# Optimization experiments

Hardware: AMD Instinct MI355X
Metric: run time of the kernel (lower is better)

Reference implementation:

```python
import jax, jax.numpy as jnp
import numpy as np


def _rel_coords_log(ws: int) -> np.ndarray:
    # matches torch.meshgrid default indexing='ij'
    idx = np.arange(ws, dtype=np.float32)
    coords = np.stack(np.meshgrid(idx, idx, indexing='ij'), axis=0).reshape(2, -1)  # [2, ws^2]
    rel = coords[:, :, None] - coords[:, None, :]  # [2, T, T]
    rel = rel.transpose(1, 2, 0).reshape(-1, 2)    # [T*T, 2]
    return np.sign(rel) * np.log1p(np.abs(rel))


def setup_inputs() -> dict:
    key = jax.random.key(0)
    ks = jax.random.split(key, 9)
    B, C, Hd, ws, meta_h = 256, 256, 8, 16, 256
    s = 1.0 / np.sqrt(C)
    return {
        'x': jax.random.normal(ks[0], (B, C, ws, ws), dtype=jnp.float32),
        'w_qkv': jax.random.normal(ks[1], (3 * C, C), dtype=jnp.float32) * s,
        'b_qkv': jax.random.normal(ks[2], (3 * C,), dtype=jnp.float32) * 0.01,
        'w_proj': jax.random.normal(ks[3], (C, C), dtype=jnp.float32) * s,
        'b_proj': jax.random.normal(ks[4], (C,), dtype=jnp.float32) * 0.01,
        'mw1': jax.random.normal(ks[5], (meta_h, 2), dtype=jnp.float32) * 0.5,
        'mb1': jax.random.normal(ks[6], (meta_h,), dtype=jnp.float32) * 0.01,
        'mw2': jax.random.normal(ks[7], (Hd, meta_h), dtype=jnp.float32) * (1.0 / np.sqrt(meta_h)),
        'mb2': jax.random.normal(ks[8], (Hd,), dtype=jnp.float32) * 0.01,
        'tau': jnp.ones((1, Hd, 1, 1), dtype=jnp.float32),
    }


def reference(x, w_qkv, b_qkv, w_proj, b_proj, mw1, mb1, mw2, mb2, tau):
    B, C, H, W = x.shape
    T = H * W
    nh = tau.shape[1]
    hd = C // nh
    # [B, C, H, W] -> [B, T, C]
    xt = x.reshape(B, C, T).transpose(0, 2, 1)
    qkv = xt @ w_qkv.T + b_qkv                                  # [B, T, 3C]
    qkv = qkv.reshape(B, T, 3, nh, hd).transpose(2, 0, 3, 1, 4)  # [3, B, nh, T, hd]
    q, k, v = qkv[0], qkv[1], qkv[2]
    # cosine similarity attention
    qn = jnp.linalg.norm(q, axis=-1, keepdims=True)              # [B, nh, T, 1]
    kn = jnp.linalg.norm(k, axis=-1, keepdims=True)
    denom = jnp.maximum(qn * kn.transpose(0, 1, 3, 2), 1e-6)
    scores = jnp.einsum('bhqd,bhkd->bhqk', q, k) / denom
    scores = scores / jnp.maximum(tau, 0.01)
    # MLP relative position bias (static coords)
    rc = jnp.asarray(_rel_coords_log(H))                          # [T*T, 2]
    bias = jax.nn.relu(rc @ mw1.T + mb1) @ mw2.T + mb2            # [T*T, nh]
    bias = bias.T.reshape(nh, T, T)
    scores = scores + bias[None]
    attn = jax.nn.softmax(scores, axis=-1)
    out = jnp.einsum('bhqk,bhkd->bhqd', attn, v)                  # [B, nh, T, hd]
    out = out.transpose(0, 2, 1, 3).reshape(B, T, C)
    out = out @ w_proj.T + b_proj
    return out.transpose(0, 2, 1).reshape(B, C, H, W)
```

## Files before the change

kernel.cpp:

```cpp
#include <hip/hip_runtime.h>
#include <math.h>

#define Cc 256
#define NH 8
#define HD 32
#define Tt 256
#define MH 256
#define TBL 961

typedef _Float16 f16;
typedef f16 f16x4 __attribute__((ext_vector_type(4)));
typedef f16 f16x8 __attribute__((ext_vector_type(8)));
typedef float f32x4 __attribute__((ext_vector_type(4)));

__device__ __forceinline__ f16x8 ld8(const f16* base, int row, int kc) {
  return *(const f16x8*)&base[row * 32 + ((kc ^ ((row >> 2) & 3)) << 3)];
}
__device__ __forceinline__ void st8(f16* base, int row, int kc, f16x8 v) {
  *(f16x8*)&base[row * 32 + ((kc ^ ((row >> 2) & 3)) << 3)] = v;
}
__device__ __forceinline__ int sidx(int row, int col) {
  return row * 32 + (((col >> 3) ^ ((row >> 2) & 3)) << 3) + (col & 7);
}
__device__ __forceinline__ int vsidx(int d, int t) {
  return d * 256 + (((t >> 3) ^ (d & 7)) << 3) + (t & 7);
}
__device__ __forceinline__ f16x8 vld8(const f16* base, int d, int tch) {
  return *(const f16x8*)&base[d * 256 + ((tch ^ (d & 7)) << 3)];
}

__global__ __launch_bounds__(256) void prep_kernel(
    const float* __restrict__ mw1, const float* __restrict__ mb1,
    const float* __restrict__ mw2, const float* __restrict__ mb2,
    const float* __restrict__ w_proj, float* __restrict__ table,
    float* __restrict__ tablemax, f16* __restrict__ wpf) {
  int blk = blockIdx.x, tid = threadIdx.x;
  if (blk >= NH) {
    int base = (blk - NH) * 2048 + tid * 8;
    f16x8 v;
#pragma unroll
    for (int u = 0; u < 8; u++) v[u] = (f16)w_proj[base + u];
    *(f16x8*)&wpf[base] = v;
    return;
  }
  __shared__ float s_w1a[MH], s_w1b[MH], s_b1[MH], s_w2[MH];
  __shared__ float red[256];
  for (int i = tid; i < MH; i += 256) {
    s_w1a[i] = mw1[2 * i];
    s_w1b[i] = mw1[2 * i + 1];
    s_b1[i] = mb1[i];
    s_w2[i] = mw2[blk * MH + i];
  }
  __syncthreads();
  float lmax = -1e30f;
  float b2 = mb2[blk];
  for (int idx = tid; idx < TBL; idx += 256) {
    float fdi = (float)(idx / 31 - 15);
    float fdj = (float)(idx % 31 - 15);
    float d0 = (fdi > 0.f ? 1.f : (fdi < 0.f ? -1.f : 0.f)) * log1pf(fabsf(fdi));
    float d1 = (fdj > 0.f ? 1.f : (fdj < 0.f ? -1.f : 0.f)) * log1pf(fabsf(fdj));
    float o = b2;
    for (int m = 0; m < MH; m++) {
      float hid = fmaxf(fmaf(d0, s_w1a[m], fmaf(d1, s_w1b[m], s_b1[m])), 0.f);
      o = fmaf(hid, s_w2[m], o);
    }
    table[blk * TBL + idx] = o;
    lmax = fmaxf(lmax, o);
  }
  red[tid] = lmax;
  __syncthreads();
  for (int s = 128; s > 0; s >>= 1) {
    if (tid < s) red[tid] = fmaxf(red[tid], red[tid + s]);
    __syncthreads();
  }
  if (tid == 0) tablemax[blk] = red[0];
}

__global__ __launch_bounds__(512, 4) void fused_attn(
    const float* __restrict__ x, const float* __restrict__ w_qkv,
    const float* __restrict__ b_qkv, const float* __restrict__ table,
    const float* __restrict__ tablemax, const float* __restrict__ tau,
    f16* __restrict__ attnH) {
  __shared__ __align__(16) char smem[68352];
  f16* Qa = (f16*)smem;
  f16* Ka = (f16*)(smem + 16384);
  f16* Vt = (f16*)(smem + 32768);
  f16* Pspare = (f16*)(smem + 49152);
  float* tbv = (float*)(smem + 51456);
  float* rs = (float*)(smem + 67328);
  f16* Xa = (f16*)smem;
  f16* Wa = (f16*)(smem + 16384);

  int tid = threadIdx.x;
  int bh = blockIdx.x, b = bh >> 3, h = bh & 7;
  int wv = tid >> 6, ln = tid & 63, lq = ln >> 4, lm = ln & 15;

  const float LOG2E = 1.4426950408889634f;
  float rtau = 1.0f / fmaxf(tau[h], 0.01f);
  float tmaxh = tablemax[h];

  for (int idx = tid; idx < 31 * 32; idx += 512) {
    int di_ = idx >> 5, c = idx & 31;
    float4 v;
    float* vp = (float*)&v;
#pragma unroll
    for (int u = 0; u < 4; u++) {
      int dj = c - u;
      dj = dj < 0 ? 0 : (dj > 30 ? 30 : dj);
      vp[u] = (table[h * TBL + di_ * 31 + dj] - tmaxh - rtau * 1.0001f) * LOG2E;
    }
    *(float4*)&tbv[idx * 4] = v;
  }

  float bj[6];
#pragma unroll
  for (int nt = 0; nt < 6; nt++) {
    int n = nt * 16 + lm;
    int row = ((n >> 5) << 8) + (h << 5) + (n & 31);
    bj[nt] = b_qkv[row];
  }

  f32x4 acc[2][6] = {};
  for (int c0 = 0; c0 < Cc; c0 += 32) {
    {
      int t = tid & 255, cg = tid >> 8;
      f16x8 v0, v1;
#pragma unroll
      for (int cc = 0; cc < 8; cc++)
        v0[cc] = (f16)x[(size_t)b * 65536 + (size_t)(c0 + cg * 16 + cc) * 256 + t];
#pragma unroll
      for (int cc = 0; cc < 8; cc++)
        v1[cc] = (f16)x[(size_t)b * 65536 + (size_t)(c0 + cg * 16 + 8 + cc) * 256 + t];
      st8(Xa, t, cg * 2 + 0, v0);
      st8(Xa, t, cg * 2 + 1, v1);
    }
    if (tid < 384) {
      int n = tid >> 2, ck = tid & 3;
      int row = ((n >> 5) << 8) + (h << 5) + (n & 31);
      const float* wp = w_qkv + (size_t)row * Cc + c0 + ck * 8;
      f16x8 v;
#pragma unroll
      for (int u = 0; u < 8; u++) v[u] = (f16)wp[u];
      st8(Wa, n, ck, v);
    }
    __syncthreads();
    f16x8 af[2], bf[6];
#pragma unroll
    for (int e = 0; e < 2; e++) af[e] = ld8(Xa, wv * 32 + e * 16 + lm, lq);
#pragma unroll
    for (int nt = 0; nt < 6; nt++) bf[nt] = ld8(Wa, nt * 16 + lm, lq);
#pragma unroll
    for (int e = 0; e < 2; e++)
#pragma unroll
      for (int nt = 0; nt < 6; nt++)
        acc[e][nt] = __builtin_amdgcn_mfma_f32_16x16x32_f16(af[e], bf[nt],
                                                            acc[e][nt], 0, 0, 0);
    __syncthreads();
  }

#pragma unroll
  for (int e = 0; e < 2; e++) {
#pragma unroll
    for (int nt = 0; nt < 6; nt++) {
      int d = (nt & 1) * 16 + lm;
#pragma unroll
      for (int r = 0; r < 4; r++) {
        int t = wv * 32 + e * 16 + lq * 4 + r;
        f16 v = (f16)(acc[e][nt][r] + bj[nt]);
        if (nt < 2)      Qa[sidx(t, d)] = v;
        else if (nt < 4) Ka[sidx(t, d)] = v;
        else             Vt[vsidx(d, t)] = v;
      }
    }
  }
  __syncthreads();

  if (tid < 256) {
    int t = tid;
    float s = 0.f;
    f16x8 v[4];
#pragma unroll
    for (int ck = 0; ck < 4; ck++) {
      v[ck] = *(f16x8*)&Qa[t * 32 + ck * 8];
#pragma unroll
      for (int u = 0; u < 8; u++) { float f = (float)v[ck][u]; s = fmaf(f, f, s); }
    }
    float sc_ = rsqrtf(s) * rtau * LOG2E;
#pragma unroll
    for (int ck = 0; ck < 4; ck++) {
      f16x8 o;
#pragma unroll
      for (int u = 0; u < 8; u++) o[u] = (f16)((float)v[ck][u] * sc_);
      *(f16x8*)&Qa[t * 32 + ck * 8] = o;
    }
  } else {
    int t = tid - 256;
    float s = 0.f;
    f16x8 v[4];
#pragma unroll
    for (int ck = 0; ck < 4; ck++) {
      v[ck] = *(f16x8*)&Ka[t * 32 + ck * 8];
#pragma unroll
      for (int u = 0; u < 8; u++) { float f = (float)v[ck][u]; s = fmaf(f, f, s); }
    }
    float sc_ = rsqrtf(s);
#pragma unroll
    for (int ck = 0; ck < 4; ck++) {
      f16x8 o;
#pragma unroll
      for (int u = 0; u < 8; u++) o[u] = (f16)((float)v[ck][u] * sc_);
      *(f16x8*)&Ka[t * 32 + ck * 8] = o;
    }
  }
  __syncthreads();

  f16x8 qf[2];
#pragma unroll
  for (int e = 0; e < 2; e++) qf[e] = ld8(Qa, wv * 32 + e * 16 + lm, lq);
  __syncthreads();

  f16* Pme = (wv < 7) ? (Qa + wv * 1152) : Pspare;
  int c0l = lm - lq * 4 + 15;
  const float4* tbp = (const float4*)tbv;
  float lsum[2] = {0.f, 0.f};
  f32x4 acco[2][2] = {};
  int dibase = wv * 2 + 15;

  for (int n0 = 0; n0 < Tt; n0 += 32) {
    f16x8 kf[2];
#pragma unroll
    for (int nt = 0; nt < 2; nt++) kf[nt] = ld8(Ka, n0 + nt * 16 + lm, lq);
    f32x4 zero = {0.f, 0.f, 0.f, 0.f};
    f32x4 sc[2][2];
#pragma unroll
    for (int e = 0; e < 2; e++)
#pragma unroll
      for (int nt = 0; nt < 2; nt++)
        sc[e][nt] = __builtin_amdgcn_mfma_f32_16x16x32_f16(kf[nt], qf[e], zero,
                                                           0, 0, 0);
#pragma unroll
    for (int e = 0; e < 2; e++) {
#pragma unroll
      for (int nt = 0; nt < 2; nt++) {
        int di_ = dibase + e - (n0 >> 4) - nt;
        float4 bv = tbp[di_ * 32 + c0l];
        const float* bvp = (const float*)&bv;
        f16x4 pv;
#pragma unroll
        for (int r = 0; r < 4; r++) {
          float p = exp2f(sc[e][nt][r] + bvp[r]);
          lsum[e] += p;
          pv[r] = (f16)p;
        }
        *(f16x4*)&Pme[(e * 16 + lm) * 36 + nt * 16 + lq * 4] = pv;
      }
    }
    asm volatile("s_waitcnt lgkmcnt(0)" ::: "memory");
    f16x8 pf[2], vf[2];
#pragma unroll
    for (int e = 0; e < 2; e++) {
      f16x4 p0 = *(f16x4*)&Pme[(e * 16 + lm) * 36 + lq * 8];
      f16x4 p1 = *(f16x4*)&Pme[(e * 16 + lm) * 36 + lq * 8 + 4];
      pf[e] = __builtin_shufflevector(p0, p1, 0, 1, 2, 3, 4, 5, 6, 7);
    }
#pragma unroll
    for (int dt = 0; dt < 2; dt++)
      vf[dt] = vld8(Vt, dt * 16 + lm, (n0 >> 3) + lq);
#pragma unroll
    for (int e = 0; e < 2; e++)
#pragma unroll
      for (int dt = 0; dt < 2; dt++)
        acco[e][dt] = __builtin_amdgcn_mfma_f32_16x16x32_f16(pf[e], vf[dt],
                                                             acco[e][dt], 0, 0, 0);
  }

#pragma unroll
  for (int e = 0; e < 2; e++) {
    float v = lsum[e];
    v += __shfl_xor(v, 16);
    v += __shfl_xor(v, 32);
    lsum[e] = v;
  }
  if (ln < 16) {
    rs[wv * 32 + lm] = lsum[0];
    rs[wv * 32 + 16 + lm] = lsum[1];
  }
  asm volatile("s_waitcnt lgkmcnt(0)" ::: "memory");
#pragma unroll
  for (int e = 0; e < 2; e++)
#pragma unroll
    for (int r = 0; r < 4; r++) {
      float rl = __builtin_amdgcn_rcpf(rs[wv * 32 + e * 16 + lq * 4 + r]);
      int q = wv * 32 + e * 16 + lq * 4 + r;
#pragma unroll
      for (int dt = 0; dt < 2; dt++) {
        int d = dt * 16 + lm;
        attnH[((size_t)b * Tt + q) * Cc + h * HD + d] =
            (f16)(acco[e][dt][r] * rl);
      }
    }
}

__global__ __launch_bounds__(256, 4) void proj_gemm(
    const f16* __restrict__ A, const f16* __restrict__ wf,
    const float* __restrict__ bp, float* __restrict__ out) {
  __shared__ __align__(16) f16 Af[128 * 72];
  __shared__ __align__(16) f16 Wsh[128 * 72];
  __shared__ float sB[128];
  int tid = threadIdx.x;
  int row0 = blockIdx.x * 128;
  int n0g = blockIdx.y * 128;
  int b = row0 >> 8, t0 = row0 & 255;
  int wv = tid >> 6, ln = tid & 63, lq = ln >> 4, lm = ln & 15;
  int cw = (wv & 1) * 64, tw = (wv >> 1) * 64;

  if (tid < 128) sB[tid] = bp[n0g + tid];

  f32x4 acc[4][4] = {};
  for (int k0 = 0; k0 < Cc; k0 += 64) {
#pragma unroll
    for (int p = 0; p < 4; p++) {
      int idx = p * 256 + tid;
      int row = idx >> 3, ch = idx & 7;
      f16x8 v = *(const f16x8*)&A[(size_t)(row0 + row) * Cc + k0 + ch * 8];
      *(f16x8*)&Af[row * 72 + ch * 8] = v;
    }
#pragma unroll
    for (int p = 0; p < 4; p++) {
      int idx = p * 256 + tid;
      int row = idx >> 3, ch = idx & 7;
      f16x8 v = *(const f16x8*)&wf[(size_t)(n0g + row) * Cc + k0 + ch * 8];
      *(f16x8*)&Wsh[row * 72 + ch * 8] = v;
    }
    __syncthreads();
#pragma unroll
    for (int kk = 0; kk < 2; kk++) {
      f16x8 wfr[4], af[4];
#pragma unroll
      for (int i = 0; i < 4; i++)
        wfr[i] = *(f16x8*)&Wsh[(cw + i * 16 + lm) * 72 + (kk * 4 + lq) * 8];
#pragma unroll
      for (int j = 0; j < 4; j++)
        af[j] = *(f16x8*)&Af[(tw + j * 16 + lm) * 72 + (kk * 4 + lq) * 8];
#pragma unroll
      for (int i = 0; i < 4; i++)
#pragma unroll
        for (int j = 0; j < 4; j++)
          acc[i][j] = __builtin_amdgcn_mfma_f32_16x16x32_f16(wfr[i], af[j],
                                                             acc[i][j], 0, 0, 0);
    }
    __syncthreads();
  }

#pragma unroll
  for (int i = 0; i < 4; i++)
#pragma unroll
    for (int r = 0; r < 4; r++) {
      int crl = cw + i * 16 + lq * 4 + r;
      float bias = sB[crl];
#pragma unroll
      for (int j = 0; j < 4; j++) {
        int tcl = tw + j * 16 + lm;
        out[(size_t)b * 65536 + (size_t)(n0g + crl) * 256 + t0 + tcl] =
            acc[i][j][r] + bias;
      }
    }
}

extern "C" void kernel_launch(void* const* d_in, const int* in_sizes, int n_in,
                              void* d_out, int out_size, void* d_ws,
                              size_t ws_size, hipStream_t stream) {
  const float* x = (const float*)d_in[0];
  const float* w_qkv = (const float*)d_in[1];
  const float* b_qkv = (const float*)d_in[2];
  const float* w_proj = (const float*)d_in[3];
  const float* b_proj = (const float*)d_in[4];
  const float* mw1 = (const float*)d_in[5];
  const float* mb1 = (const float*)d_in[6];
  const float* mw2 = (const float*)d_in[7];
  const float* mb2 = (const float*)d_in[8];
  const float* tau = (const float*)d_in[9];
  float* out = (float*)d_out;

  const size_t NEEDED = (size_t)(TBL * NH + NH) * 4 + (size_t)65536 * 2 +
                        (size_t)256 * NH * Tt * HD * 2;
  if (ws_size < NEEDED) return;

  float* table = (float*)d_ws;
  float* tablemax = table + TBL * NH;
  f16* wpf = (f16*)(tablemax + NH);
  f16* attnH = wpf + 65536;

  prep_kernel<<<40, 256, 0, stream>>>(mw1, mb1, mw2, mb2, w_proj, table,
                                      tablemax, wpf);
  fused_attn<<<256 * NH, 512, 0, stream>>>(x, w_qkv, b_qkv, table, tablemax,
                                           tau, attnH);
  dim3 g3(512, 2);
  proj_gemm<<<g3, 256, 0, stream>>>(attnH, wpf, b_proj, out);
}
```

Baseline: 278.9 us.

## Precompute bias table globally, reorder attention blocks by head, restructure projection GEMM

The per-head shifted bias table is now built once in the prep kernel and written to global memory. The attention kernel reads it from global/L2 instead of rebuilding it in LDS, which shrinks LDS use. Attention blocks are remapped so consecutive blocks share a head, which improves L2 reuse of weights and table. The projection GEMM is rewritten so one 512-thread block per batch keeps the full A tile in swizzled LDS and streams the weights directly from global memory. The risk is global-load latency in the inner softmax loop and only 256 blocks for the GEMM.

```diff
diff --git a/kernel.cpp b/kernel.cpp
--- a/kernel.cpp
+++ b/kernel.cpp
@@ -32,8 +32,8 @@
 __global__ __launch_bounds__(256) void prep_kernel(
     const float* __restrict__ mw1, const float* __restrict__ mb1,
     const float* __restrict__ mw2, const float* __restrict__ mb2,
-    const float* __restrict__ w_proj, float* __restrict__ table,
-    float* __restrict__ tablemax, f16* __restrict__ wpf) {
+    const float* __restrict__ w_proj, const float* __restrict__ tau,
+    float* __restrict__ tbvg, f16* __restrict__ wpf) {
   int blk = blockIdx.x, tid = threadIdx.x;
   if (blk >= NH) {
     int base = (blk - NH) * 2048 + tid * 8;
@@ -44,7 +44,9 @@
     return;
   }
   __shared__ float s_w1a[MH], s_w1b[MH], s_b1[MH], s_w2[MH];
+  __shared__ float tb[TBL];
   __shared__ float red[256];
+  const float LOG2E = 1.4426950408889634f;
   for (int i = tid; i < MH; i += 256) {
     s_w1a[i] = mw1[2 * i];
     s_w1b[i] = mw1[2 * i + 1];
@@ -64,7 +66,7 @@
       float hid = fmaxf(fmaf(d0, s_w1a[m], fmaf(d1, s_w1b[m], s_b1[m])), 0.f);
       o = fmaf(hid, s_w2[m], o);
     }
-    table[blk * TBL + idx] = o;
+    tb[idx] = o;
     lmax = fmaxf(lmax, o);
   }
   red[tid] = lmax;
@@ -73,44 +75,42 @@
     if (tid < s) red[tid] = fmaxf(red[tid], red[tid + s]);
     __syncthreads();
   }
-  if (tid == 0) tablemax[blk] = red[0];
+  float rtau = 1.0f / fmaxf(tau[blk], 0.01f);
+  float shift = red[0] + rtau * 1.0001f;
+  __syncthreads();
+  for (int idx = tid; idx < 31 * 32; idx += 256) {
+    int di_ = idx >> 5, c = idx & 31;
+    float4 v;
+    float* vp = (float*)&v;
+#pragma unroll
+    for (int u = 0; u < 4; u++) {
+      int dj = c - u;
+      dj = dj < 0 ? 0 : (dj > 30 ? 30 : dj);
+      vp[u] = (tb[di_ * 31 + dj] - shift) * LOG2E;
+    }
+    *(float4*)&tbvg[(size_t)(blk * 992 + idx) * 4] = v;
+  }
 }
 
 __global__ __launch_bounds__(512, 4) void fused_attn(
     const float* __restrict__ x, const float* __restrict__ w_qkv,
-    const float* __restrict__ b_qkv, const float* __restrict__ table,
-    const float* __restrict__ tablemax, const float* __restrict__ tau,
-    f16* __restrict__ attnH) {
-  __shared__ __align__(16) char smem[68352];
+    const float* __restrict__ b_qkv, const float* __restrict__ tbvg,
+    const float* __restrict__ tau, f16* __restrict__ attnH) {
+  __shared__ __align__(16) char smem[52480];
   f16* Qa = (f16*)smem;
   f16* Ka = (f16*)(smem + 16384);
   f16* Vt = (f16*)(smem + 32768);
   f16* Pspare = (f16*)(smem + 49152);
-  float* tbv = (float*)(smem + 51456);
-  float* rs = (float*)(smem + 67328);
+  float* rs = (float*)(smem + 51456);
   f16* Xa = (f16*)smem;
   f16* Wa = (f16*)(smem + 16384);
 
   int tid = threadIdx.x;
-  int bh = blockIdx.x, b = bh >> 3, h = bh & 7;
+  int bh = blockIdx.x, b = bh & 255, h = bh >> 8;
   int wv = tid >> 6, ln = tid & 63, lq = ln >> 4, lm = ln & 15;
 
   const float LOG2E = 1.4426950408889634f;
   float rtau = 1.0f / fmaxf(tau[h], 0.01f);
-  float tmaxh = tablemax[h];
-
-  for (int idx = tid; idx < 31 * 32; idx += 512) {
-    int di_ = idx >> 5, c = idx & 31;
-    float4 v;
-    float* vp = (float*)&v;
-#pragma unroll
-    for (int u = 0; u < 4; u++) {
-      int dj = c - u;
-      dj = dj < 0 ? 0 : (dj > 30 ? 30 : dj);
-      vp[u] = (table[h * TBL + di_ * 31 + dj] - tmaxh - rtau * 1.0001f) * LOG2E;
-    }
-    *(float4*)&tbv[idx * 4] = v;
-  }
 
   float bj[6];
 #pragma unroll
@@ -221,12 +221,19 @@
 
   f16* Pme = (wv < 7) ? (Qa + wv * 1152) : Pspare;
   int c0l = lm - lq * 4 + 15;
-  const float4* tbp = (const float4*)tbv;
+  const float4* tbph = (const float4*)tbvg + h * 992;
   float lsum[2] = {0.f, 0.f};
   f32x4 acco[2][2] = {};
   int dibase = wv * 2 + 15;
 
   for (int n0 = 0; n0 < Tt; n0 += 32) {
+    float4 bv[2][2];
+#pragma unroll
+    for (int e = 0; e < 2; e++)
+#pragma unroll
+      for (int nt = 0; nt < 2; nt++)
+        bv[e][nt] = tbph[(dibase + e - (n0 >> 4) - nt) * 32 + c0l];
+
     f16x8 kf[2];
 #pragma unroll
     for (int nt = 0; nt < 2; nt++) kf[nt] = ld8(Ka, n0 + nt * 16 + lm, lq);
@@ -242,9 +249,7 @@
     for (int e = 0; e < 2; e++) {
 #pragma unroll
       for (int nt = 0; nt < 2; nt++) {
-        int di_ = dibase + e - (n0 >> 4) - nt;
-        float4 bv = tbp[di_ * 32 + c0l];
-        const float* bvp = (const float*)&bv;
+        const float* bvp = (const float*)&bv[e][nt];
         f16x4 pv;
 #pragma unroll
         for (int r = 0; r < 4; r++) {
@@ -301,70 +306,67 @@
     }
 }
 
-__global__ __launch_bounds__(256, 4) void proj_gemm(
+__global__ __launch_bounds__(512, 2) void proj_gemm(
     const f16* __restrict__ A, const f16* __restrict__ wf,
     const float* __restrict__ bp, float* __restrict__ out) {
-  __shared__ __align__(16) f16 Af[128 * 72];
-  __shared__ __align__(16) f16 Wsh[128 * 72];
-  __shared__ float sB[128];
+  __shared__ __align__(16) f16 As[256 * 256];
+  __shared__ float sB[256];
   int tid = threadIdx.x;
-  int row0 = blockIdx.x * 128;
-  int n0g = blockIdx.y * 128;
-  int b = row0 >> 8, t0 = row0 & 255;
+  int b = blockIdx.x;
+  int row0 = b * 256;
   int wv = tid >> 6, ln = tid & 63, lq = ln >> 4, lm = ln & 15;
-  int cw = (wv & 1) * 64, tw = (wv >> 1) * 64;
-
-  if (tid < 128) sB[tid] = bp[n0g + tid];
-
-  f32x4 acc[4][4] = {};
-  for (int k0 = 0; k0 < Cc; k0 += 64) {
-#pragma unroll
-    for (int p = 0; p < 4; p++) {
-      int idx = p * 256 + tid;
-      int row = idx >> 3, ch = idx & 7;
-      f16x8 v = *(const f16x8*)&A[(size_t)(row0 + row) * Cc + k0 + ch * 8];
-      *(f16x8*)&Af[row * 72 + ch * 8] = v;
-    }
-#pragma unroll
-    for (int p = 0; p < 4; p++) {
-      int idx = p * 256 + tid;
-      int row = idx >> 3, ch = idx & 7;
-      f16x8 v = *(const f16x8*)&wf[(size_t)(n0g + row) * Cc + k0 + ch * 8];
-      *(f16x8*)&Wsh[row * 72 + ch * 8] = v;
-    }
-    __syncthreads();
-#pragma unroll
-    for (int kk = 0; kk < 2; kk++) {
-      f16x8 wfr[4], af[4];
-#pragma unroll
-      for (int i = 0; i < 4; i++)
-        wfr[i] = *(f16x8*)&Wsh[(cw + i * 16 + lm) * 72 + (kk * 4 + lq) * 8];
-#pragma unroll
-      for (int j = 0; j < 4; j++)
-        af[j] = *(f16x8*)&Af[(tw + j * 16 + lm) * 72 + (kk * 4 + lq) * 8];
-#pragma unroll
-      for (int i = 0; i < 4; i++)
-#pragma unroll
-        for (int j = 0; j < 4; j++)
-          acc[i][j] = __builtin_amdgcn_mfma_f32_16x16x32_f16(wfr[i], af[j],
-                                                             acc[i][j], 0, 0, 0);
-    }
-    __syncthreads();
-  }
-
-#pragma unroll
-  for (int i = 0; i < 4; i++)
-#pragma unroll
-    for (int r = 0; r < 4; r++) {
-      int crl = cw + i * 16 + lq * 4 + r;
-      float bias = sB[crl];
-#pragma unroll
-      for (int j = 0; j < 4; j++) {
-        int tcl = tw + j * 16 + lm;
-        out[(size_t)b * 65536 + (size_t)(n0g + crl) * 256 + t0 + tcl] =
-            acc[i][j][r] + bias;
-      }
-    }
+
+  if (tid < 256) sB[tid] = bp[tid];
+
+#pragma unroll
+  for (int i = 0; i < 16; i++) {
+    int p = i * 512 + tid;
+    int row = p >> 5, pr = p & 31;
+    int ch = (pr & 24) | ((pr & 7) ^ (row & 7));
+    f16x8 v = *(const f16x8*)&A[((size_t)row0 + row) * 256 + ch * 8];
+    *(f16x8*)&As[p * 8] = v;
+  }
+  __syncthreads();
+
+  int tw = wv * 32;
+#pragma unroll
+  for (int half = 0; half < 2; half++) {
+    int c0 = half * 128;
+    f32x4 acc[2][8] = {};
+    for (int kit = 0; kit < 8; kit++) {
+      f16x8 wfr[8];
+#pragma unroll
+      for (int nt = 0; nt < 8; nt++)
+        wfr[nt] = *(const f16x8*)&wf[(size_t)(c0 + nt * 16 + lm) * 256 +
+                                     kit * 32 + lq * 8];
+      f16x8 af[2];
+#pragma unroll
+      for (int e = 0; e < 2; e++) {
+        int row = tw + e * 16 + lm;
+        int ch = kit * 4 + lq;
+        int pos = row * 32 + ((ch & 24) | ((ch & 7) ^ (row & 7)));
+        af[e] = *(const f16x8*)&As[pos * 8];
+      }
+#pragma unroll
+      for (int e = 0; e < 2; e++)
+#pragma unroll
+        for (int nt = 0; nt < 8; nt++)
+          acc[e][nt] = __builtin_amdgcn_mfma_f32_16x16x32_f16(wfr[nt], af[e],
+                                                              acc[e][nt], 0, 0, 0);
+    }
+#pragma unroll
+    for (int nt = 0; nt < 8; nt++)
+#pragma unroll
+      for (int r = 0; r < 4; r++) {
+        int c = c0 + nt * 16 + lq * 4 + r;
+        float bias = sB[c];
+#pragma unroll
+        for (int e = 0; e < 2; e++) {
+          int t = tw + e * 16 + lm;
+          out[(size_t)b * 65536 + (size_t)c * 256 + t] = acc[e][nt][r] + bias;
+        }
+      }
+  }
 }
 
 extern "C" void kernel_launch(void* const* d_in, const int* in_sizes, int n_in,
@@ -382,19 +384,16 @@
   const float* tau = (const float*)d_in[9];
   float* out = (float*)d_out;
 
-  const size_t NEEDED = (size_t)(TBL * NH + NH) * 4 + (size_t)65536 * 2 +
+  const size_t NEEDED = (size_t)NH * 992 * 16 + (size_t)65536 * 2 +
                         (size_t)256 * NH * Tt * HD * 2;
   if (ws_size < NEEDED) return;
 
-  float* table = (float*)d_ws;
-  float* tablemax = table + TBL * NH;
-  f16* wpf = (f16*)(tablemax + NH);
+  float* tbvg = (float*)d_ws;
+  f16* wpf = (f16*)((char*)d_ws + (size_t)NH * 992 * 16);
   f16* attnH = wpf + 65536;
 
-  prep_kernel<<<40, 256, 0, stream>>>(mw1, mb1, mw2, mb2, w_proj, table,
-                                      tablemax, wpf);
-  fused_attn<<<256 * NH, 512, 0, stream>>>(x, w_qkv, b_qkv, table, tablemax,
-                                           tau, attnH);
-  dim3 g3(512, 2);
-  proj_gemm<<<g3, 256, 0, stream>>>(attnH, wpf, b_proj, out);
-}
+  prep_kernel<<<40, 256, 0, stream>>>(mw1, mb1, mw2, mb2, w_proj, tau, tbvg,
+                                      wpf);
+  fused_attn<<<256 * NH, 512, 0, stream>>>(x, w_qkv, b_qkv, tbvg, tau, attnH);
+  proj_gemm<<<256, 512, 0, stream>>>(attnH, wpf, b_proj, out);
+}
```

Measured after the change: 286.5 us. 1.03x slower.
